# Kernel optimization log

Measured on AMD Instinct MI355X. Metric: run time of the kernel, lower is better.

## Reference

```python
import jax, jax.numpy as jnp
import numpy as np

NUM_DIM = 2
N, P, Q, C = 2048, 2048, 64, 2

def _mlp(x, layers, activate_final):
    n = len(layers)
    for i, (w, b) in enumerate(layers):
        x = x @ w + b
        if i < n - 1 or activate_final:
            x = jnp.tanh(x)
    return x

def setup_inputs() -> dict:
    key = jax.random.key(0)
    ks = jax.random.split(key, 24)
    s = 0.3  # param scale for numerical sanity
    return {
        "phase_coords": jax.random.normal(ks[0], (N, 2 * NUM_DIM), jnp.float32),
        "boundary_coords": jax.random.normal(ks[1], (N, 2 * NUM_DIM), jnp.float32),
        "coeff_position": jax.random.normal(ks[2], (P, NUM_DIM), jnp.float32),
        "coeff_values": jax.random.uniform(ks[3], (P, C), jnp.float32),
        "scattering_kernel_coords": jax.random.normal(ks[4], (Q, NUM_DIM), jnp.float32),
        "scattering_kernel": jax.random.uniform(ks[5], (Q,), jnp.float32),
        "velocity_weights": jax.random.uniform(ks[6], (Q,), jnp.float32) / Q,
        "attn_w1": s * jax.random.normal(ks[7], (6, 32), jnp.float32),
        "attn_b1": jnp.zeros((32,), jnp.float32),
        "attn_w2": s * jax.random.normal(ks[8], (32, 32), jnp.float32),
        "attn_b2": jnp.zeros((32,), jnp.float32),
        "attn_w3": s * jax.random.normal(ks[9], (32, 1), jnp.float32),
        "attn_b3": jnp.zeros((1,), jnp.float32),
        "green_w1": s * jax.random.normal(ks[10], (4 * NUM_DIM + C, 64), jnp.float32),
        "green_b1": jnp.zeros((64,), jnp.float32),
        "green_w2": s * jax.random.normal(ks[11], (64, 64), jnp.float32),
        "green_b2": jnp.zeros((64,), jnp.float32),
        "green_w3": s * jax.random.normal(ks[12], (64, 64), jnp.float32),
        "green_b3": jnp.zeros((64,), jnp.float32),
        "res_w": s * jax.random.normal(ks[13], (64, 64), jnp.float32),
        "res_b": jnp.zeros((64,), jnp.float32),
        "final_w": s * jax.random.normal(ks[14], (64, 1), jnp.float32),
        "final_b": jnp.zeros((1,), jnp.float32),
    }

def reference(phase_coords, boundary_coords, coeff_position, coeff_values,
              scattering_kernel_coords, scattering_kernel, velocity_weights,
              attn_w1, attn_b1, attn_w2, attn_b2, attn_w3, attn_b3,
              green_w1, green_b1, green_w2, green_b2, green_w3, green_b3,
              res_w, res_b, final_w, final_b):
    attn_layers = [(attn_w1, attn_b1), (attn_w2, attn_b2), (attn_w3, attn_b3)]
    green_layers = [(green_w1, green_b1), (green_w2, green_b2), (green_w3, green_b3)]

    x, v = phase_coords[:, :NUM_DIM], phase_coords[:, NUM_DIM:]     # (N,2),(N,2)
    xp, vp = boundary_coords[:, :NUM_DIM], boundary_coords[:, NUM_DIM:]

    # --- CoefficientNet: MLP attention logits + geometric mask + softmax over P ---
    ang = v / jnp.sqrt(jnp.sum(v**2, -1, keepdims=True) + 1e-16)     # (N,2)
    rel = x[:, None, :] - coeff_position[None, :, :]                 # (N,P,2)
    dist = jnp.sqrt(jnp.sum(rel**2, -1) + 1e-16)                     # (N,P)
    pos_loc = jnp.einsum('npd,nd->np', rel, ang)                     # (N,P)
    ang_loc = pos_loc / (dist + 1e-8)
    frames = jnp.stack([ang_loc, pos_loc], -1)                       # (N,P,2)
    coords = jnp.concatenate([x, v], -1)                             # (N,4)
    qk = jnp.concatenate(
        [jnp.broadcast_to(coords[:, None, :], (coords.shape[0], frames.shape[1], coords.shape[1])), frames], -1)  # (N,P,6)
    logits = _mlp(qk, attn_layers, False)[..., 0]                    # (N,P)
    logits = jnp.where(pos_loc > 0, logits, -1e30)
    aw = jax.nn.softmax(logits, axis=-1)
    coeff = jnp.exp(-(aw @ coeff_values))                            # (N,C)

    # --- GreenFunctionBlock (coefficients only depend on (x,v)) ---
    g0 = jnp.exp(_mlp(jnp.concatenate([x, v, xp, vp, coeff], -1), green_layers, True))  # (N,64)

    # --- res block depth=1: quadrature over velocity_prime (argnum=3) ---
    w_quad = (1.0 - scattering_kernel) * velocity_weights            # (Q,)
    Nn = x.shape[0]; Qq = scattering_kernel_coords.shape[0]
    base = jnp.concatenate([x, v, xp], -1)                           # (N,6)
    inp_q = jnp.concatenate([
        jnp.broadcast_to(base[:, None, :], (Nn, Qq, base.shape[1])),
        jnp.broadcast_to(scattering_kernel_coords[None, :, :], (Nn, Qq, NUM_DIM)),
        jnp.broadcast_to(coeff[:, None, :], (Nn, Qq, coeff.shape[1])),
    ], -1)                                                           # (N,Q,10)
    gq = jnp.exp(_mlp(inp_q, green_layers, True))                    # (N,Q,64)
    quad = jnp.einsum('nqh,q->nh', gq, w_quad)                       # (N,64)
    res = jnp.tanh(quad @ res_w + res_b)                             # widths[-1:], activate_final
    out = g0 + res
    return out @ final_w + final_b                                   # (N,1)
```

## Files before the change

kernel.cpp:

```cpp
#include <hip/hip_runtime.h>

#define NN 2048
#define PP 2048
#define QQ 64
#define GR_ROWS 4
#define GR_SLOTS 80
#define GR_MT 5

typedef __attribute__((ext_vector_type(8))) short short8;
typedef __attribute__((ext_vector_type(4))) float f32x4;
typedef __attribute__((ext_vector_type(4))) unsigned u32x4;

union V4 { u32x4 u; short8 s; };

#if __has_builtin(__builtin_amdgcn_exp2f)
#define EXP2(x) __builtin_amdgcn_exp2f(x)
#else
#define EXP2(x) exp2f(x)
#endif

__device__ __forceinline__ float fast_rcp(float x) { return __builtin_amdgcn_rcpf(x); }

__device__ __forceinline__ float fast_tanh(float x) {
    float t = EXP2(x * 2.885390082f);
    return 1.0f - 2.0f * __builtin_amdgcn_rcpf(t + 1.0f);
}

__device__ __forceinline__ unsigned cvt_pk_bf16(float lo, float hi) {
    unsigned r;
    asm("v_cvt_pk_bf16_f32 %0, %1, %2" : "=v"(r) : "v"(lo), "v"(hi));
    return r;
}
__device__ __forceinline__ unsigned short bf16_bits(float f) {
    unsigned u = __builtin_bit_cast(unsigned, f);
    u += 0x7FFFu + ((u >> 16) & 1u);
    return (unsigned short)(u >> 16);
}

__global__ __launch_bounds__(256) void attn_kernel(
    const float* __restrict__ pc, const float* __restrict__ cp,
    const float* __restrict__ cv,
    const float* __restrict__ w1, const float* __restrict__ b1,
    const float* __restrict__ w2, const float* __restrict__ b2,
    const float* __restrict__ w3, const float* __restrict__ b3,
    float* __restrict__ coeff_out)
{
    __shared__ float2 scpc[PP];
    __shared__ unsigned short slist[PP];
    __shared__ float sred[16];
    __shared__ int scount;

    const int n = blockIdx.x;
    const int t = threadIdx.x;
    const int wid  = t >> 6;
    const int lane = t & 63;
    const int c15  = lane & 15;
    const int kg   = lane >> 4;
    const int k0   = kg * 8;

    const float b3v = b3[0];

    if (t == 0) scount = 0;

    const float x0 = pc[n*4+0], x1 = pc[n*4+1];
    const float v0 = pc[n*4+2], v1 = pc[n*4+3];
    const float rinv = __builtin_amdgcn_rsqf(v0*v0 + v1*v1 + 1e-16f);
    const float a0 = v0 * rinv, a1 = v1 * rinv;

    union BF { short8 s8; unsigned u[4]; } B0, B1;
    #pragma unroll
    for (int j2 = 0; j2 < 4; ++j2) {
        const int ka = k0 + 2*j2, kb = ka + 1;
        B0.u[j2] = cvt_pk_bf16(w2[ka*32 + c15],      w2[kb*32 + c15]);
        B1.u[j2] = cvt_pk_bf16(w2[ka*32 + c15 + 16], w2[kb*32 + c15 + 16]);
    }
    float b2a[4], b2b[4], w3a[4], w3b[4];
    #pragma unroll
    for (int r = 0; r < 4; ++r) {
        b2a[r] = b2[kg*4 + r];      b2b[r] = b2[16 + kg*4 + r];
        w3a[r] = w3[kg*4 + r];      w3b[r] = w3[16 + kg*4 + r];
    }
    float cfrag[8], w1a[8], w1b[8];
    #pragma unroll
    for (int j = 0; j < 8; ++j) {
        const int k = k0 + j;
        float c = b1[k];
        c = fmaf(x0, w1[0*32+k], c);
        c = fmaf(x1, w1[1*32+k], c);
        c = fmaf(v0, w1[2*32+k], c);
        c = fmaf(v1, w1[3*32+k], c);
        cfrag[j] = c;
        w1a[j] = w1[4*32+k];
        w1b[j] = w1[5*32+k];
    }
    __syncthreads();

    #pragma unroll 1
    for (int i = 0; i < PP/256; ++i) {
        const int p = i*256 + t;
        const float2 cpp = ((const float2*)cp)[p];
        const float r0 = x0 - cpp.x;
        const float r1 = x1 - cpp.y;
        const float pos = fmaf(r0, a0, r1*a1);
        const bool f = pos > 0.0f;
        const unsigned long long mask = __ballot(f);
        int base = 0;
        if (lane == 0 && mask) base = atomicAdd(&scount, __popcll(mask));
        base = __shfl(base, 0);
        if (f) {
            const int idx = base + __popcll(mask & ((1ull << lane) - 1ull));
            const float dist = sqrtf(r0*r0 + r1*r1 + 1e-16f);
            const float angl = pos * fast_rcp(dist + 1e-8f);
            slist[idx] = (unsigned short)p;
            scpc[idx] = make_float2(angl, pos);
        }
    }
    __syncthreads();
    const int M  = scount;
    const int Mt = (M + 15) >> 4;

    #pragma unroll 2
    for (int tile = wid; tile < Mt; tile += 4) {
        const int li = tile*16 + c15;
        const float2 ap = scpc[li < M ? li : 0];
        const float angl = ap.x, pos = ap.y;

        union AF { short8 s8; unsigned u[4]; } H;
        #pragma unroll
        for (int j2 = 0; j2 < 4; ++j2) {
            const float ha = fast_tanh(fmaf(angl, w1a[2*j2+0], fmaf(pos, w1b[2*j2+0], cfrag[2*j2+0])));
            const float hb = fast_tanh(fmaf(angl, w1a[2*j2+1], fmaf(pos, w1b[2*j2+1], cfrag[2*j2+1])));
            H.u[j2] = cvt_pk_bf16(ha, hb);
        }

        f32x4 acca = {b2a[0], b2a[1], b2a[2], b2a[3]};
        f32x4 accb = {b2b[0], b2b[1], b2b[2], b2b[3]};
        acca = __builtin_amdgcn_mfma_f32_16x16x32_bf16(B0.s8, H.s8, acca, 0, 0, 0);
        accb = __builtin_amdgcn_mfma_f32_16x16x32_bf16(B1.s8, H.s8, accb, 0, 0, 0);

        float lg = 0.0f;
        #pragma unroll
        for (int r = 0; r < 4; ++r) {
            lg = fmaf(fast_tanh(acca[r]), w3a[r], lg);
            lg = fmaf(fast_tanh(accb[r]), w3b[r], lg);
        }
        lg += __shfl_xor(lg, 16);
        lg += __shfl_xor(lg, 32);

        if (kg == 0 && li < M) scpc[li].x = lg + b3v;
    }
    __syncthreads();

    float m = -3.4e38f;
    if (M > 0)
        for (int i = t; i < M; i += 256) m = fmaxf(m, scpc[i].x);
    #pragma unroll
    for (int off = 32; off; off >>= 1) m = fmaxf(m, __shfl_xor(m, off));
    if (lane == 0) sred[wid] = m;
    __syncthreads();
    m = fmaxf(fmaxf(sred[0], sred[1]), fmaxf(sred[2], sred[3]));

    float s = 0.0f, q0 = 0.0f, q1 = 0.0f;
    if (M > 0) {
        #pragma unroll 2
        for (int i = t; i < M; i += 256) {
            const float e = EXP2((scpc[i].x - m) * 1.44269504f);
            const float2 cvv = ((const float2*)cv)[slist[i]];
            s += e;
            q0 = fmaf(e, cvv.x, q0);
            q1 = fmaf(e, cvv.y, q1);
        }
    } else {
        for (int i = t; i < PP; i += 256) {
            const float2 cvv = ((const float2*)cv)[i];
            s += 1.0f; q0 += cvv.x; q1 += cvv.y;
        }
    }
    #pragma unroll
    for (int off = 32; off; off >>= 1) {
        s  += __shfl_xor(s, off);
        q0 += __shfl_xor(q0, off);
        q1 += __shfl_xor(q1, off);
    }
    __syncthreads();
    if (lane == 0) {
        sred[4 + wid*3 + 0] = s;
        sred[4 + wid*3 + 1] = q0;
        sred[4 + wid*3 + 2] = q1;
    }
    __syncthreads();
    if (t == 0) {
        float S = 0.0f, Q0 = 0.0f, Q1 = 0.0f;
        #pragma unroll
        for (int w = 0; w < 4; ++w) {
            S  += sred[4 + w*3 + 0];
            Q0 += sred[4 + w*3 + 1];
            Q1 += sred[4 + w*3 + 2];
        }
        const float invS = fast_rcp(S);
        coeff_out[n*2+0] = __expf(-Q0 * invS);
        coeff_out[n*2+1] = __expf(-Q1 * invS);
    }
}

__global__ __launch_bounds__(256) void green_kernel(
    const float* __restrict__ pc,  const float* __restrict__ bc,
    const float* __restrict__ skc, const float* __restrict__ sk,
    const float* __restrict__ vw,
    const float* __restrict__ gw1, const float* __restrict__ gb1,
    const float* __restrict__ gw2, const float* __restrict__ gb2,
    const float* __restrict__ gw3, const float* __restrict__ gb3,
    const float* __restrict__ rw,  const float* __restrict__ rb,
    const float* __restrict__ fw,  const float* __restrict__ fb,
    const float* __restrict__ coeff,
    float* __restrict__ out)
{
    __shared__ unsigned short sinA[GR_ROWS*GR_SLOTS*16];
    __shared__ unsigned short shb[4][16*64];
    __shared__ float swq[GR_SLOTS];
    __shared__ float sg0[4][64];
    __shared__ float squad[4][64];

    const int t = threadIdx.x;
    const int w = t >> 6, lane = t & 63;
    const int c15 = lane & 15, kg = lane >> 4;
    const int n0 = blockIdx.x * GR_ROWS;

    V4 Bw1[4], Bw2[2][4], Bw3[2][4];
    #pragma unroll
    for (int nt = 0; nt < 4; ++nt) {
        const int col = c15 + nt*16;
        #pragma unroll
        for (int j2 = 0; j2 < 4; ++j2) {
            const int ka = kg*8 + 2*j2, kb = ka + 1;
            const float va = (ka < 10) ? gw1[ka*64 + col] : 0.0f;
            const float vb = (kb < 10) ? gw1[kb*64 + col] : 0.0f;
            Bw1[nt].u[j2] = cvt_pk_bf16(va, vb);
        }
        #pragma unroll
        for (int kt = 0; kt < 2; ++kt) {
            #pragma unroll
            for (int j2 = 0; j2 < 4; ++j2) {
                const int ka = kt*32 + kg*8 + 2*j2, kb = ka + 1;
                Bw2[kt][nt].u[j2] = cvt_pk_bf16(gw2[ka*64 + col], gw2[kb*64 + col]);
                Bw3[kt][nt].u[j2] = cvt_pk_bf16(gw3[ka*64 + col], gw3[kb*64 + col]);
            }
        }
    }
    float b1c[4], b2c[4], b3c[4];
    #pragma unroll
    for (int nt = 0; nt < 4; ++nt) {
        b1c[nt] = gb1[c15 + nt*16];
        b2c[nt] = gb2[c15 + nt*16];
        b3c[nt] = gb3[c15 + nt*16];
    }

    for (int row = t; row < GR_ROWS*GR_SLOTS; row += 256) {
        const int nl = row / GR_SLOTS;
        const int s  = row - nl*GR_SLOTS;
        const int n  = n0 + nl;
        u32x4 lo = {0u,0u,0u,0u}, hi = {0u,0u,0u,0u};
        if (s <= 64) {
            const float X0 = pc[n*4+0], X1 = pc[n*4+1];
            const float V0 = pc[n*4+2], V1 = pc[n*4+3];
            const float XP0 = bc[n*4+0], XP1 = bc[n*4+1];
            float I6, I7;
            if (s == 64) { I6 = bc[n*4+2]; I7 = bc[n*4+3]; }
            else         { I6 = skc[s*2+0]; I7 = skc[s*2+1]; }
            const float C0 = coeff[n*2+0], C1 = coeff[n*2+1];
            lo[0] = cvt_pk_bf16(X0, X1);
            lo[1] = cvt_pk_bf16(V0, V1);
            lo[2] = cvt_pk_bf16(XP0, XP1);
            lo[3] = cvt_pk_bf16(I6, I7);
            hi[0] = cvt_pk_bf16(C0, C1);
        }
        ((u32x4*)sinA)[row*2 + 0] = lo;
        ((u32x4*)sinA)[row*2 + 1] = hi;
    }
    if (t < GR_SLOTS)
        swq[t] = (t < QQ) ? (1.0f - sk[t]) * vw[t] : 0.0f;
    __syncthreads();

    unsigned short* hb = &shb[w][0];
    float qacc[4] = {0.f, 0.f, 0.f, 0.f};

    #pragma unroll 1
    for (int T = 0; T < GR_MT; ++T) {
        const int rm = w*GR_SLOTS + T*16 + c15;
        V4 A1; A1.u = (u32x4){0u,0u,0u,0u};
        if (kg < 2) A1.u = ((u32x4*)sinA)[rm*2 + kg];

        f32x4 acc1[4];
        #pragma unroll
        for (int nt = 0; nt < 4; ++nt) {
            f32x4 a = {b1c[nt], b1c[nt], b1c[nt], b1c[nt]};
            acc1[nt] = __builtin_amdgcn_mfma_f32_16x16x32_bf16(A1.s, Bw1[nt].s, a, 0, 0, 0);
        }
        #pragma unroll
        for (int nt = 0; nt < 4; ++nt) {
            #pragma unroll
            for (int r = 0; r < 4; ++r) {
                const int rl = kg*4 + r;
                hb[rl*64 + ((c15 + nt*16) ^ ((rl&7)<<3))] = bf16_bits(fast_tanh(acc1[nt][r]));
            }
        }
        V4 A2[2];
        #pragma unroll
        for (int kt = 0; kt < 2; ++kt)
            A2[kt].u = ((u32x4*)hb)[(c15*64 + ((kt*32 + kg*8) ^ ((c15&7)<<3))) >> 3];
        f32x4 acc2[4];
        #pragma unroll
        for (int nt = 0; nt < 4; ++nt) {
            f32x4 a = {b2c[nt], b2c[nt], b2c[nt], b2c[nt]};
            a = __builtin_amdgcn_mfma_f32_16x16x32_bf16(A2[0].s, Bw2[0][nt].s, a, 0, 0, 0);
            acc2[nt] = __builtin_amdgcn_mfma_f32_16x16x32_bf16(A2[1].s, Bw2[1][nt].s, a, 0, 0, 0);
        }
        #pragma unroll
        for (int nt = 0; nt < 4; ++nt) {
            #pragma unroll
            for (int r = 0; r < 4; ++r) {
                const int rl = kg*4 + r;
                hb[rl*64 + ((c15 + nt*16) ^ ((rl&7)<<3))] = bf16_bits(fast_tanh(acc2[nt][r]));
            }
        }
        V4 A3[2];
        #pragma unroll
        for (int kt = 0; kt < 2; ++kt)
            A3[kt].u = ((u32x4*)hb)[(c15*64 + ((kt*32 + kg*8) ^ ((c15&7)<<3))) >> 3];
        f32x4 acc3[4];
        #pragma unroll
        for (int nt = 0; nt < 4; ++nt) {
            f32x4 a = {b3c[nt], b3c[nt], b3c[nt], b3c[nt]};
            a = __builtin_amdgcn_mfma_f32_16x16x32_bf16(A3[0].s, Bw3[0][nt].s, a, 0, 0, 0);
            acc3[nt] = __builtin_amdgcn_mfma_f32_16x16x32_bf16(A3[1].s, Bw3[1][nt].s, a, 0, 0, 0);
        }
        #pragma unroll
        for (int r = 0; r < 4; ++r) {
            const int s = T*16 + kg*4 + r;
            const float wq = swq[s];
            #pragma unroll
            for (int nt = 0; nt < 4; ++nt) {
                const float g = __expf(fast_tanh(acc3[nt][r]));
                qacc[nt] = fmaf(wq, g, qacc[nt]);
                if (T == GR_MT-1 && kg == 0 && r == 0) sg0[w][c15 + nt*16] = g;
            }
        }
    }

    #pragma unroll
    for (int nt = 0; nt < 4; ++nt) {
        qacc[nt] += __shfl_xor(qacc[nt], 16);
        qacc[nt] += __shfl_xor(qacc[nt], 32);
    }
    if (kg == 0) {
        #pragma unroll
        for (int nt = 0; nt < 4; ++nt) squad[w][c15 + nt*16] = qacc[nt];
    }

    const int k = lane;
    float r0a = rb[k], r1a = 0.f, r2a = 0.f, r3a = 0.f;
    #pragma unroll
    for (int j = 0; j < 64; j += 4) {
        const float4 qd = *(const float4*)&squad[w][j];
        r0a = fmaf(qd.x, rw[(j+0)*64 + k], r0a);
        r1a = fmaf(qd.y, rw[(j+1)*64 + k], r1a);
        r2a = fmaf(qd.z, rw[(j+2)*64 + k], r2a);
        r3a = fmaf(qd.w, rw[(j+3)*64 + k], r3a);
    }
    const float resv = fast_tanh((r0a + r1a) + (r2a + r3a));
    float term = (sg0[w][k] + resv) * fw[k];
    #pragma unroll
    for (int off = 32; off; off >>= 1) term += __shfl_xor(term, off);
    if (lane == 0) out[n0 + w] = term + fb[0];
}

extern "C" void kernel_launch(void* const* d_in, const int* in_sizes, int n_in,
                              void* d_out, int out_size, void* d_ws, size_t ws_size,
                              hipStream_t stream) {
    const float* pc  = (const float*)d_in[0];
    const float* bc  = (const float*)d_in[1];
    const float* cp  = (const float*)d_in[2];
    const float* cv  = (const float*)d_in[3];
    const float* skc = (const float*)d_in[4];
    const float* sk  = (const float*)d_in[5];
    const float* vw  = (const float*)d_in[6];
    const float* aw1 = (const float*)d_in[7];
    const float* ab1 = (const float*)d_in[8];
    const float* aw2 = (const float*)d_in[9];
    const float* ab2 = (const float*)d_in[10];
    const float* aw3 = (const float*)d_in[11];
    const float* ab3 = (const float*)d_in[12];
    const float* gw1 = (const float*)d_in[13];
    const float* gb1 = (const float*)d_in[14];
    const float* gw2 = (const float*)d_in[15];
    const float* gb2 = (const float*)d_in[16];
    const float* gw3 = (const float*)d_in[17];
    const float* gb3 = (const float*)d_in[18];
    const float* rw  = (const float*)d_in[19];
    const float* rb  = (const float*)d_in[20];
    const float* fw  = (const float*)d_in[21];
    const float* fb  = (const float*)d_in[22];

    float* coeff = (float*)d_ws;
    float* outp  = (float*)d_out;

    attn_kernel<<<NN, 256, 0, stream>>>(pc, cp, cv, aw1, ab1, aw2, ab2, aw3, ab3, coeff);
    green_kernel<<<NN/GR_ROWS, 256, 0, stream>>>(pc, bc, skc, sk, vw,
                                                 gw1, gb1, gw2, gb2, gw3, gb3,
                                                 rw, rb, fw, fb, coeff, outp);
}
```

Measured before the change: 84.24 us.

## Split attention into a logits kernel and a softmax kernel through global workspace

Replaces the single per-row attention kernel with two kernels. The first uses four 128-thread blocks per row, each wave compacting its positive-projection points and evaluating the MLP with bf16 MFMA; it writes logits, or -1e30 for masked points, to a global NxP buffer. The second does a per-row softmax-weighted reduction of the coefficient values. This spreads the work over more, smaller blocks, at the cost of writing and re-reading a 16 MB logits buffer plus one extra launch. It falls back to the old kernel when the workspace is too small.

```diff
diff --git a/kernel.cpp b/kernel.cpp
--- a/kernel.cpp
+++ b/kernel.cpp
@@ -35,6 +35,171 @@
     unsigned u = __builtin_bit_cast(unsigned, f);
     u += 0x7FFFu + ((u >> 16) & 1u);
     return (unsigned short)(u >> 16);
+}
+
+__global__ __launch_bounds__(128) void attn_logits_kernel(
+    const float* __restrict__ pc, const float* __restrict__ cp,
+    const float* __restrict__ w1, const float* __restrict__ b1,
+    const float* __restrict__ w2, const float* __restrict__ b2,
+    const float* __restrict__ w3, const float* __restrict__ b3,
+    float* __restrict__ logits_g)
+{
+    __shared__ float2 sap[2][256];
+    __shared__ unsigned short sidx[2][256];
+
+    const int t = threadIdx.x;
+    const int w = t >> 6, lane = t & 63;
+    const int c15 = lane & 15, kg = lane >> 4;
+    const int k0 = kg * 8;
+    const int n  = blockIdx.x >> 2;
+    const int p0 = (blockIdx.x & 3) * 512 + w * 256;
+
+    const float b3v = b3[0];
+    const float x0 = pc[n*4+0], x1 = pc[n*4+1];
+    const float v0 = pc[n*4+2], v1 = pc[n*4+3];
+    const float rinv = __builtin_amdgcn_rsqf(v0*v0 + v1*v1 + 1e-16f);
+    const float a0 = v0 * rinv, a1 = v1 * rinv;
+
+    float* __restrict__ lrow = logits_g + (size_t)n * PP;
+
+    int cnt = 0;
+    #pragma unroll
+    for (int i = 0; i < 4; ++i) {
+        const int p = p0 + i*64 + lane;
+        const float2 cpp = ((const float2*)cp)[p];
+        const float r0 = x0 - cpp.x;
+        const float r1 = x1 - cpp.y;
+        const float pos = fmaf(r0, a0, r1*a1);
+        const bool f = pos > 0.0f;
+        if (!f) lrow[p] = -1e30f;
+        const unsigned long long mask = __ballot(f);
+        if (f) {
+            const int idx = cnt + __popcll(mask & ((1ull << lane) - 1ull));
+            const float dist = sqrtf(r0*r0 + r1*r1 + 1e-16f);
+            const float angl = pos * fast_rcp(dist + 1e-8f);
+            sap[w][idx]  = make_float2(angl, pos);
+            sidx[w][idx] = (unsigned short)p;
+        }
+        cnt += __popcll(mask);
+    }
+
+    union BF { short8 s8; unsigned u[4]; } B0, B1;
+    #pragma unroll
+    for (int j2 = 0; j2 < 4; ++j2) {
+        const int ka = k0 + 2*j2, kb = ka + 1;
+        B0.u[j2] = cvt_pk_bf16(w2[ka*32 + c15],      w2[kb*32 + c15]);
+        B1.u[j2] = cvt_pk_bf16(w2[ka*32 + c15 + 16], w2[kb*32 + c15 + 16]);
+    }
+    float b2a[4], b2b[4], w3a[4], w3b[4];
+    #pragma unroll
+    for (int r = 0; r < 4; ++r) {
+        b2a[r] = b2[kg*4 + r];      b2b[r] = b2[16 + kg*4 + r];
+        w3a[r] = w3[kg*4 + r];      w3b[r] = w3[16 + kg*4 + r];
+    }
+    float cfrag[8], w1a[8], w1b[8];
+    #pragma unroll
+    for (int j = 0; j < 8; ++j) {
+        const int k = k0 + j;
+        float c = b1[k];
+        c = fmaf(x0, w1[0*32+k], c);
+        c = fmaf(x1, w1[1*32+k], c);
+        c = fmaf(v0, w1[2*32+k], c);
+        c = fmaf(v1, w1[3*32+k], c);
+        cfrag[j] = c;
+        w1a[j] = w1[4*32+k];
+        w1b[j] = w1[5*32+k];
+    }
+
+    const int nt = (cnt + 15) >> 4;
+    #pragma unroll 2
+    for (int tile = 0; tile < nt; ++tile) {
+        const int li = tile*16 + c15;
+        const float2 ap = sap[w][li < cnt ? li : 0];
+        const float angl = ap.x, pos = ap.y;
+
+        union AF { short8 s8; unsigned u[4]; } H;
+        #pragma unroll
+        for (int j2 = 0; j2 < 4; ++j2) {
+            const float ha = fast_tanh(fmaf(angl, w1a[2*j2+0], fmaf(pos, w1b[2*j2+0], cfrag[2*j2+0])));
+            const float hb = fast_tanh(fmaf(angl, w1a[2*j2+1], fmaf(pos, w1b[2*j2+1], cfrag[2*j2+1])));
+            H.u[j2] = cvt_pk_bf16(ha, hb);
+        }
+
+        f32x4 acca = {b2a[0], b2a[1], b2a[2], b2a[3]};
+        f32x4 accb = {b2b[0], b2b[1], b2b[2], b2b[3]};
+        acca = __builtin_amdgcn_mfma_f32_16x16x32_bf16(B0.s8, H.s8, acca, 0, 0, 0);
+        accb = __builtin_amdgcn_mfma_f32_16x16x32_bf16(B1.s8, H.s8, accb, 0, 0, 0);
+
+        float lg = 0.0f;
+        #pragma unroll
+        for (int r = 0; r < 4; ++r) {
+            lg = fmaf(fast_tanh(acca[r]), w3a[r], lg);
+            lg = fmaf(fast_tanh(accb[r]), w3b[r], lg);
+        }
+        lg += __shfl_xor(lg, 16);
+        lg += __shfl_xor(lg, 32);
+
+        if (kg == 0 && li < cnt) lrow[sidx[w][li]] = lg + b3v;
+    }
+}
+
+__global__ __launch_bounds__(256) void attn_softmax_kernel(
+    const float* __restrict__ logits_g, const float* __restrict__ cv,
+    float* __restrict__ coeff_out)
+{
+    __shared__ float sred[16];
+    const int n = blockIdx.x;
+    const int t = threadIdx.x;
+    const int wid = t >> 6, lane = t & 63;
+    const float* __restrict__ lrow = logits_g + (size_t)n * PP;
+
+    float m = -3.4e38f;
+    float lg[PP/256];
+    #pragma unroll
+    for (int i = 0; i < PP/256; ++i) {
+        lg[i] = lrow[i*256 + t];
+        m = fmaxf(m, lg[i]);
+    }
+    #pragma unroll
+    for (int off = 32; off; off >>= 1) m = fmaxf(m, __shfl_xor(m, off));
+    if (lane == 0) sred[wid] = m;
+    __syncthreads();
+    m = fmaxf(fmaxf(sred[0], sred[1]), fmaxf(sred[2], sred[3]));
+
+    float s = 0.0f, q0 = 0.0f, q1 = 0.0f;
+    #pragma unroll
+    for (int i = 0; i < PP/256; ++i) {
+        const float e = EXP2((lg[i] - m) * 1.44269504f);
+        const float2 cvv = ((const float2*)cv)[i*256 + t];
+        s += e;
+        q0 = fmaf(e, cvv.x, q0);
+        q1 = fmaf(e, cvv.y, q1);
+    }
+    #pragma unroll
+    for (int off = 32; off; off >>= 1) {
+        s  += __shfl_xor(s, off);
+        q0 += __shfl_xor(q0, off);
+        q1 += __shfl_xor(q1, off);
+    }
+    __syncthreads();
+    if (lane == 0) {
+        sred[4 + wid*3 + 0] = s;
+        sred[4 + wid*3 + 1] = q0;
+        sred[4 + wid*3 + 2] = q1;
+    }
+    __syncthreads();
+    if (t == 0) {
+        float S = 0.0f, Q0 = 0.0f, Q1 = 0.0f;
+        #pragma unroll
+        for (int w = 0; w < 4; ++w) {
+            S  += sred[4 + w*3 + 0];
+            Q0 += sred[4 + w*3 + 1];
+            Q1 += sred[4 + w*3 + 2];
+        }
+        const float invS = fast_rcp(S);
+        coeff_out[n*2+0] = __expf(-Q0 * invS);
+        coeff_out[n*2+1] = __expf(-Q1 * invS);
+    }
 }
 
 __global__ __launch_bounds__(256) void attn_kernel(
@@ -404,7 +569,15 @@
     float* coeff = (float*)d_ws;
     float* outp  = (float*)d_out;
 
-    attn_kernel<<<NN, 256, 0, stream>>>(pc, cp, cv, aw1, ab1, aw2, ab2, aw3, ab3, coeff);
+    const size_t need = (size_t)NN*2*sizeof(float) + (size_t)NN*PP*sizeof(float);
+    if (ws_size >= need) {
+        float* logits = (float*)((char*)d_ws + (size_t)NN*2*sizeof(float));
+        attn_logits_kernel<<<NN*4, 128, 0, stream>>>(pc, cp, aw1, ab1, aw2, ab2, aw3, ab3,
+                                                     logits);
+        attn_softmax_kernel<<<NN, 256, 0, stream>>>(logits, cv, coeff);
+    } else {
+        attn_kernel<<<NN, 256, 0, stream>>>(pc, cp, cv, aw1, ab1, aw2, ab2, aw3, ab3, coeff);
+    }
     green_kernel<<<NN/GR_ROWS, 256, 0, stream>>>(pc, bc, skc, sk, vw,
                                                  gw1, gb1, gw2, gb2, gw3, gb3,
                                                  rw, rb, fw, fb, coeff, outp);
```

Result: no change. 84.98 us (+0.9%).

## Make attention softmax wave-local with static logit bound and 512 threads

Applied to the files above, without the earlier changes.

The attention kernel now uses 8 waves per block. Each wave compacts its own 256-point slice into private shared memory instead of contending on a shared atomic counter, and it no longer waits on block-wide barriers between compaction, MLP and reduction. The softmax max pass is replaced by a fixed upper bound on the logits, b3 plus the sum of |w3|, which holds because tanh outputs lie in [-1,1]. This lets exp and the weighted sums fuse into the MLP tile loop. The cost is possible underflow if real logits sit far below the bound, plus a serial fallback loop for the empty case.

```diff
diff --git a/kernel.cpp b/kernel.cpp
--- a/kernel.cpp
+++ b/kernel.cpp
@@ -37,7 +37,7 @@
     return (unsigned short)(u >> 16);
 }
 
-__global__ __launch_bounds__(256) void attn_kernel(
+__global__ __launch_bounds__(512) void attn_kernel(
     const float* __restrict__ pc, const float* __restrict__ cp,
     const float* __restrict__ cv,
     const float* __restrict__ w1, const float* __restrict__ b1,
@@ -45,27 +45,46 @@
     const float* __restrict__ w3, const float* __restrict__ b3,
     float* __restrict__ coeff_out)
 {
-    __shared__ float2 scpc[PP];
-    __shared__ unsigned short slist[PP];
-    __shared__ float sred[16];
-    __shared__ int scount;
-
-    const int n = blockIdx.x;
+    __shared__ float2 sap[8][272];
+    __shared__ unsigned short sidx[8][272];
+    __shared__ float sred[24];
+
     const int t = threadIdx.x;
-    const int wid  = t >> 6;
-    const int lane = t & 63;
-    const int c15  = lane & 15;
-    const int kg   = lane >> 4;
-    const int k0   = kg * 8;
+    const int w = t >> 6, lane = t & 63;
+    const int c15 = lane & 15, kg = lane >> 4;
+    const int k0 = kg * 8;
+    const int n  = blockIdx.x;
+    const int p0 = w * 256;
 
     const float b3v = b3[0];
-
-    if (t == 0) scount = 0;
-
     const float x0 = pc[n*4+0], x1 = pc[n*4+1];
     const float v0 = pc[n*4+2], v1 = pc[n*4+3];
     const float rinv = __builtin_amdgcn_rsqf(v0*v0 + v1*v1 + 1e-16f);
     const float a0 = v0 * rinv, a1 = v1 * rinv;
+
+    int cnt = 0;
+    #pragma unroll
+    for (int i = 0; i < 4; ++i) {
+        const int p = p0 + i*64 + lane;
+        const float2 cpp = ((const float2*)cp)[p];
+        const float r0 = x0 - cpp.x;
+        const float r1 = x1 - cpp.y;
+        const float pos = fmaf(r0, a0, r1*a1);
+        const bool f = pos > 0.0f;
+        const unsigned long long mask = __ballot(f);
+        if (f) {
+            const int idx = cnt + __popcll(mask & ((1ull << lane) - 1ull));
+            const float dist = sqrtf(r0*r0 + r1*r1 + 1e-16f);
+            const float angl = pos * fast_rcp(dist + 1e-8f);
+            sap[w][idx]  = make_float2(angl, pos);
+            sidx[w][idx] = (unsigned short)p;
+        }
+        cnt += __popcll(mask);
+    }
+    if (lane < 16) {
+        sap[w][cnt + lane]  = make_float2(0.0f, 0.0f);
+        sidx[w][cnt + lane] = 0;
+    }
 
     union BF { short8 s8; unsigned u[4]; } B0, B1;
     #pragma unroll
@@ -93,45 +112,31 @@
         w1a[j] = w1[4*32+k];
         w1b[j] = w1[5*32+k];
     }
-    __syncthreads();
-
-    #pragma unroll 1
-    for (int i = 0; i < PP/256; ++i) {
-        const int p = i*256 + t;
-        const float2 cpp = ((const float2*)cp)[p];
-        const float r0 = x0 - cpp.x;
-        const float r1 = x1 - cpp.y;
-        const float pos = fmaf(r0, a0, r1*a1);
-        const bool f = pos > 0.0f;
-        const unsigned long long mask = __ballot(f);
-        int base = 0;
-        if (lane == 0 && mask) base = atomicAdd(&scount, __popcll(mask));
-        base = __shfl(base, 0);
-        if (f) {
-            const int idx = base + __popcll(mask & ((1ull << lane) - 1ull));
-            const float dist = sqrtf(r0*r0 + r1*r1 + 1e-16f);
-            const float angl = pos * fast_rcp(dist + 1e-8f);
-            slist[idx] = (unsigned short)p;
-            scpc[idx] = make_float2(angl, pos);
-        }
-    }
-    __syncthreads();
-    const int M  = scount;
-    const int Mt = (M + 15) >> 4;
-
+    float sw3 = 0.0f;
+    #pragma unroll
+    for (int j = 0; j < 32; ++j) sw3 += fabsf(w3[j]);
+    const float Lb = fabsf(b3v) + sw3;
+    const float C_E = (b3v - Lb) * 1.44269504f;
+
+    float s = 0.0f, q0 = 0.0f, q1 = 0.0f;
+    const int nt = (cnt + 15) >> 4;
     #pragma unroll 2
-    for (int tile = wid; tile < Mt; tile += 4) {
+    for (int tile = 0; tile < nt; ++tile) {
         const int li = tile*16 + c15;
-        const float2 ap = scpc[li < M ? li : 0];
+        const float2 ap = sap[w][li];
         const float angl = ap.x, pos = ap.y;
 
+        float pre[8], h[8];
+        #pragma unroll
+        for (int j = 0; j < 8; ++j)
+            pre[j] = fmaf(angl, w1a[j], fmaf(pos, w1b[j], cfrag[j]));
+        #pragma unroll
+        for (int j = 0; j < 8; ++j) h[j] = fast_tanh(pre[j]);
+
         union AF { short8 s8; unsigned u[4]; } H;
         #pragma unroll
-        for (int j2 = 0; j2 < 4; ++j2) {
-            const float ha = fast_tanh(fmaf(angl, w1a[2*j2+0], fmaf(pos, w1b[2*j2+0], cfrag[2*j2+0])));
-            const float hb = fast_tanh(fmaf(angl, w1a[2*j2+1], fmaf(pos, w1b[2*j2+1], cfrag[2*j2+1])));
-            H.u[j2] = cvt_pk_bf16(ha, hb);
-        }
+        for (int j2 = 0; j2 < 4; ++j2)
+            H.u[j2] = cvt_pk_bf16(h[2*j2], h[2*j2+1]);
 
         f32x4 acca = {b2a[0], b2a[1], b2a[2], b2a[3]};
         f32x4 accb = {b2b[0], b2b[1], b2b[2], b2b[3]};
@@ -147,55 +152,38 @@
         lg += __shfl_xor(lg, 16);
         lg += __shfl_xor(lg, 32);
 
-        if (kg == 0 && li < M) scpc[li].x = lg + b3v;
-    }
-    __syncthreads();
-
-    float m = -3.4e38f;
-    if (M > 0)
-        for (int i = t; i < M; i += 256) m = fmaxf(m, scpc[i].x);
-    #pragma unroll
-    for (int off = 32; off; off >>= 1) m = fmaxf(m, __shfl_xor(m, off));
-    if (lane == 0) sred[wid] = m;
-    __syncthreads();
-    m = fmaxf(fmaxf(sred[0], sred[1]), fmaxf(sred[2], sred[3]));
-
-    float s = 0.0f, q0 = 0.0f, q1 = 0.0f;
-    if (M > 0) {
-        #pragma unroll 2
-        for (int i = t; i < M; i += 256) {
-            const float e = EXP2((scpc[i].x - m) * 1.44269504f);
-            const float2 cvv = ((const float2*)cv)[slist[i]];
-            s += e;
-            q0 = fmaf(e, cvv.x, q0);
-            q1 = fmaf(e, cvv.y, q1);
-        }
-    } else {
-        for (int i = t; i < PP; i += 256) {
-            const float2 cvv = ((const float2*)cv)[i];
-            s += 1.0f; q0 += cvv.x; q1 += cvv.y;
-        }
-    }
-    #pragma unroll
-    for (int off = 32; off; off >>= 1) {
+        const bool val = (kg == 0) && (li < cnt);
+        const int pidx = (int)sidx[w][li];
+        const float2 cvv = ((const float2*)cv)[pidx];
+        const float e = val ? EXP2(fmaf(lg, 1.44269504f, C_E)) : 0.0f;
+        s += e;
+        q0 = fmaf(e, cvv.x, q0);
+        q1 = fmaf(e, cvv.y, q1);
+    }
+
+    #pragma unroll
+    for (int off = 1; off < 64; off <<= 1) {
         s  += __shfl_xor(s, off);
         q0 += __shfl_xor(q0, off);
         q1 += __shfl_xor(q1, off);
     }
-    __syncthreads();
     if (lane == 0) {
-        sred[4 + wid*3 + 0] = s;
-        sred[4 + wid*3 + 1] = q0;
-        sred[4 + wid*3 + 2] = q1;
+        sred[w*3 + 0] = s;
+        sred[w*3 + 1] = q0;
+        sred[w*3 + 2] = q1;
     }
     __syncthreads();
     if (t == 0) {
         float S = 0.0f, Q0 = 0.0f, Q1 = 0.0f;
         #pragma unroll
-        for (int w = 0; w < 4; ++w) {
-            S  += sred[4 + w*3 + 0];
-            Q0 += sred[4 + w*3 + 1];
-            Q1 += sred[4 + w*3 + 2];
+        for (int i = 0; i < 8; ++i) {
+            S  += sred[i*3 + 0];
+            Q0 += sred[i*3 + 1];
+            Q1 += sred[i*3 + 2];
+        }
+        if (!(S > 0.0f)) {
+            S = (float)PP; Q0 = 0.0f; Q1 = 0.0f;
+            for (int p = 0; p < PP; ++p) { Q0 += cv[2*p]; Q1 += cv[2*p+1]; }
         }
         const float invS = fast_rcp(S);
         coeff_out[n*2+0] = __expf(-Q0 * invS);
@@ -404,7 +392,7 @@
     float* coeff = (float*)d_ws;
     float* outp  = (float*)d_out;
 
-    attn_kernel<<<NN, 256, 0, stream>>>(pc, cp, cv, aw1, ab1, aw2, ab2, aw3, ab3, coeff);
+    attn_kernel<<<NN, 512, 0, stream>>>(pc, cp, cv, aw1, ab1, aw2, ab2, aw3, ab3, coeff);
     green_kernel<<<NN/GR_ROWS, 256, 0, stream>>>(pc, bc, skc, sk, vw,
                                                  gw1, gb1, gw2, gb2, gw3, gb3,
                                                  rw, rb, fw, fb, coeff, outp);
```

Measured after the change: 80.24 us (median of 2 runs). -4.7%, faster.
